# Optimization experiments

Measured on AMD Instinct MI355X. Metric: run time of the kernel, lower is better.

## Reference

```python
import jax, jax.numpy as jnp
import numpy as np

L, S, N, E = 1024, 1024, 16, 1024

def setup_inputs() -> dict:
    key = jax.random.key(0)
    ks = jax.random.split(key, 7)
    return {
        "query": jax.random.normal(ks[0], (L, N, E), dtype=jnp.float32),
        "key": jax.random.normal(ks[1], (S, N, E), dtype=jnp.float32),
        "value": jax.random.normal(ks[2], (S, N, E), dtype=jnp.float32),
        "q_proj_weight": jax.random.normal(ks[3], (E, E), dtype=jnp.float32) * (E ** -0.5),
        "k_proj_weight": jax.random.normal(ks[4], (E, E), dtype=jnp.float32) * (E ** -0.5),
        "v_proj_weight": jax.random.normal(ks[5], (E, E), dtype=jnp.float32) * (E ** -0.5),
        "in_proj_bias": jax.random.normal(ks[6], (3 * E,), dtype=jnp.float32) * 0.02,
    }

def reference(query, key, value, q_proj_weight, k_proj_weight, v_proj_weight, in_proj_bias):
    # query: (L, N, E); key/value: (S, N, E); single head => head_dim = E
    e = query.shape[-1]
    scaling = jnp.asarray(e, query.dtype) ** -0.5
    # F.linear(x, W, b) = x @ W.T + b
    q = (jnp.einsum("lne,fe->lnf", query, q_proj_weight) + in_proj_bias[:e]) * scaling
    k = jnp.einsum("sne,fe->snf", key, k_proj_weight) + in_proj_bias[e:2 * e]
    v = jnp.einsum("sne,fe->snf", value, v_proj_weight) + in_proj_bias[2 * e:]
    # scores: (N, L, S)
    scores = jnp.einsum("lne,sne->nls", q, k)
    attn = jax.nn.softmax(scores, axis=-1)
    # output back to (L, N, E)
    out = jnp.einsum("nls,sne->lne", attn, v)
    return out
```

## Files before the change

### kernel.cpp

```cpp
#include <hip/hip_runtime.h>
#include <stdint.h>


typedef __attribute__((ext_vector_type(8))) short bf16x8;
typedef __attribute__((ext_vector_type(4))) float f32x4;

__device__ __forceinline__ float bf2f(unsigned short u) {
    union { unsigned int i; float f; } w; w.i = ((unsigned int)u) << 16; return w.f;
}
__device__ __forceinline__ unsigned short f2bf(float f) {
    union { float f; unsigned int i; } w; w.f = f;
    unsigned int r = (w.i + 0x7FFFu + ((w.i >> 16) & 1u)) >> 16;
    return (unsigned short)r;
}

__device__ __forceinline__ void g2l16(const unsigned short* g, unsigned short* l) {
    __builtin_amdgcn_global_load_lds(
        (const __attribute__((address_space(1))) unsigned int*)g,
        (__attribute__((address_space(3))) unsigned int*)l, 16, 0, 0);
}

#define BM 256
#define BN 256
#define BK 32

template <int BIAS_MODE, typename OutT>
__global__ __launch_bounds__(512, 2) void gemm_bt2(
    const unsigned short* __restrict__ A,
    const unsigned short* __restrict__ B,
    OutT* __restrict__ C,
    const float* __restrict__ bias,
    float scale, int K,
    long lda, long ldb, long ldc,
    long aBatch, long bBatch, long cBatch,
    int gridM, int gridN)
{
    __shared__ __align__(16) unsigned short lds[65536];

    const int tid  = threadIdx.x;
    const int wave = tid >> 6;
    const int lane = tid & 63;
    const int lr   = lane & 15;
    const int q4   = lane >> 4;
    const int wm   = wave >> 2;
    const int wn   = wave & 3;

    const int p    = blockIdx.x;
    const int l    = ((p & 7) << 5) + (p >> 3);
    const int bcol = l % gridN;
    const int t2   = l / gridN;
    const int brow = t2 % gridM;
    const int bz   = t2 / gridM;

    const long m0 = (long)brow * BM;
    const long n0 = (long)bcol * BN;
    A += (long)bz * aBatch;
    B += (long)bz * bBatch;
    C += (long)bz * cBatch;

    const int tswz  = tid ^ ((tid >> 3) & 7);
    const int srow  = tswz >> 2;
    const int skoff = (tswz & 3) * 8;
    const unsigned short* aS0 = A + (m0 + srow) * lda + skoff;
    const unsigned short* aS1 = A + (m0 + 128 + srow) * lda + skoff;
    const unsigned short* bS0 = B + (n0 + srow) * ldb + skoff;
    const unsigned short* bS1 = B + (n0 + 128 + srow) * ldb + skoff;
    const int ldsW = wave * 512;

    const int myoff = (((lr << 2) | q4) ^ ((lr >> 1) & 7)) << 3;

    f32x4 acc[8][4];
    const f32x4 zero = {0.f, 0.f, 0.f, 0.f};
#pragma unroll
    for (int m = 0; m < 8; m++)
#pragma unroll
        for (int n = 0; n < 4; n++) acc[m][n] = zero;

    const int nkt = K / BK;

#pragma unroll
    for (int t = 0; t < 3; t++) {
        const long kb = (long)t * BK;
        unsigned short* base = &lds[t * 16384];
        g2l16(aS0 + kb, base + ldsW);
        g2l16(aS1 + kb, base + 4096 + ldsW);
        g2l16(bS0 + kb, base + 8192 + ldsW);
        g2l16(bS1 + kb, base + 12288 + ldsW);
    }
    asm volatile("s_waitcnt vmcnt(8)" ::: "memory");
    __builtin_amdgcn_s_barrier();

    for (int kt = 0; kt < nkt; kt++) {
        const int buf  = kt & 3;
        const int sbuf = (kt + 3) & 3;
        const int st   = (kt + 3 < nkt) ? kt + 3 : nkt - 1;
        const long kb  = (long)st * BK;
        const unsigned short* At = &lds[buf * 16384];
        const unsigned short* Bt = At + 8192;
        unsigned short* sb = &lds[sbuf * 16384];

        bf16x8 af[4], bfr[4];
#pragma unroll
        for (int m = 0; m < 4; m++)
            af[m] = *(const bf16x8*)&At[(wm * 128 + m * 16) * 32 + myoff];
#pragma unroll
        for (int n = 0; n < 4; n++)
            bfr[n] = *(const bf16x8*)&Bt[(wn * 64 + n * 16) * 32 + myoff];
        g2l16(aS0 + kb, sb + ldsW);
        g2l16(aS1 + kb, sb + 4096 + ldsW);
        __builtin_amdgcn_s_barrier();
        __builtin_amdgcn_s_setprio(1);
#pragma unroll
        for (int m = 0; m < 4; m++)
#pragma unroll
            for (int n = 0; n < 4; n++)
                acc[m][n] = __builtin_amdgcn_mfma_f32_16x16x32_bf16(
                    af[m], bfr[n], acc[m][n], 0, 0, 0);
        __builtin_amdgcn_s_setprio(0);
        __builtin_amdgcn_s_barrier();

        bf16x8 ag[4];
#pragma unroll
        for (int m = 0; m < 4; m++)
            ag[m] = *(const bf16x8*)&At[(wm * 128 + 64 + m * 16) * 32 + myoff];
        g2l16(bS0 + kb, sb + 8192 + ldsW);
        g2l16(bS1 + kb, sb + 12288 + ldsW);
        __builtin_amdgcn_s_barrier();
        __builtin_amdgcn_s_setprio(1);
#pragma unroll
        for (int m = 0; m < 4; m++)
#pragma unroll
            for (int n = 0; n < 4; n++)
                acc[4 + m][n] = __builtin_amdgcn_mfma_f32_16x16x32_bf16(
                    ag[m], bfr[n], acc[4 + m][n], 0, 0, 0);
        __builtin_amdgcn_s_setprio(0);
        asm volatile("s_waitcnt vmcnt(8)" ::: "memory");
        __builtin_amdgcn_s_barrier();
        __builtin_amdgcn_sched_barrier(0);
    }

    asm volatile("s_waitcnt vmcnt(0)" ::: "memory");
    __syncthreads();

    if constexpr (sizeof(OutT) == 2) {
#pragma unroll
        for (int m = 0; m < 8; m++)
#pragma unroll
            for (int n = 0; n < 4; n++) {
                const int col = wn * 64 + n * 16 + lr;
#pragma unroll
                for (int r = 0; r < 4; r++) {
                    const int row = wm * 128 + m * 16 + q4 * 4 + r;
                    float v = acc[m][n][r];
                    if constexpr (BIAS_MODE == 1) v += bias[n0 + col];
                    if constexpr (BIAS_MODE == 2) v += bias[m0 + row];
                    v *= scale;
                    lds[row * 256 + (col ^ (((row >> 2) & 3) << 4))] = f2bf(v);
                }
            }
        __syncthreads();
#pragma unroll
        for (int i = 0; i < 16; i++) {
            const int g   = i * 512 + tid;
            const int row = g >> 5;
            const int ch  = g & 31;
            bf16x8 v = *(const bf16x8*)&lds[row * 256 + ((ch * 8) ^ (((row >> 2) & 3) << 4))];
            *(bf16x8*)((unsigned short*)C + (m0 + row) * ldc + n0 + ch * 8) = v;
        }
    } else {
        float* fl = (float*)lds;
#pragma unroll
        for (int h = 0; h < 2; h++) {
            __syncthreads();
            if (wm == h) {
#pragma unroll
                for (int m = 0; m < 8; m++)
#pragma unroll
                    for (int n = 0; n < 4; n++) {
                        const int col = wn * 64 + n * 16 + lr;
#pragma unroll
                        for (int r = 0; r < 4; r++) {
                            const int rowh = m * 16 + q4 * 4 + r;
                            float v = acc[m][n][r];
                            if constexpr (BIAS_MODE == 1) v += bias[n0 + col];
                            if constexpr (BIAS_MODE == 2) v += bias[m0 + h * 128 + rowh];
                            v *= scale;
                            fl[rowh * 256 + (col ^ (((rowh >> 2) & 3) << 4))] = v;
                        }
                    }
            }
            __syncthreads();
#pragma unroll
            for (int i = 0; i < 16; i++) {
                const int g   = i * 512 + tid;
                const int row = g >> 6;
                const int ch  = g & 63;
                float4 v = *(const float4*)&fl[row * 256 + ((ch * 4) ^ (((row >> 2) & 3) << 4))];
                *(float4*)((float*)C + (m0 + h * 128 + row) * ldc + n0 + ch * 4) = v;
            }
        }
    }
}

__global__ __launch_bounds__(256) void cvt2_f32_bf16(
    const float* __restrict__ inA, unsigned short* __restrict__ outA, long n8A,
    const float* __restrict__ inB, unsigned short* __restrict__ outB, long n8B)
{
    const long total  = n8A + n8B;
    const long stride = (long)gridDim.x * blockDim.x;
    for (long i = (long)blockIdx.x * blockDim.x + threadIdx.x; i < total; i += stride) {
        const float* src;
        unsigned short* dst;
        long j;
        if (i < n8A) { src = inA; dst = outA; j = i; }
        else         { src = inB; dst = outB; j = i - n8A; }
        const float4* pp = (const float4*)(src + j * 8);
        float4 a = pp[0], b = pp[1];
        bf16x8 v;
        v[0] = (short)f2bf(a.x); v[1] = (short)f2bf(a.y);
        v[2] = (short)f2bf(a.z); v[3] = (short)f2bf(a.w);
        v[4] = (short)f2bf(b.x); v[5] = (short)f2bf(b.y);
        v[6] = (short)f2bf(b.z); v[7] = (short)f2bf(b.w);
        *(bf16x8*)(dst + j * 8) = v;
    }
}

__global__ __launch_bounds__(256) void softmax_rows(unsigned short* __restrict__ base)
{
    unsigned short* p = base + (long)blockIdx.x * 1024;
    const int tid = threadIdx.x;
    ushort4 u = ((const ushort4*)p)[tid];
    float x0 = bf2f(u.x), x1 = bf2f(u.y), x2 = bf2f(u.z), x3 = bf2f(u.w);
    x0 = fminf(fmaxf(x0, -1e30f), 1e30f);
    x1 = fminf(fmaxf(x1, -1e30f), 1e30f);
    x2 = fminf(fmaxf(x2, -1e30f), 1e30f);
    x3 = fminf(fmaxf(x3, -1e30f), 1e30f);

    float m = fmaxf(fmaxf(x0, x1), fmaxf(x2, x3));
#pragma unroll
    for (int o = 32; o > 0; o >>= 1) m = fmaxf(m, __shfl_xor(m, o));
    __shared__ float redm[4], reds[4];
    const int wave = tid >> 6, lane = tid & 63;
    if (lane == 0) redm[wave] = m;
    __syncthreads();
    m = fmaxf(fmaxf(redm[0], redm[1]), fmaxf(redm[2], redm[3]));

    float e0 = __expf(x0 - m), e1 = __expf(x1 - m);
    float e2 = __expf(x2 - m), e3 = __expf(x3 - m);
    float s = e0 + e1 + e2 + e3;
#pragma unroll
    for (int o = 32; o > 0; o >>= 1) s += __shfl_xor(s, o);
    if (lane == 0) reds[wave] = s;
    __syncthreads();
    s = reds[0] + reds[1] + reds[2] + reds[3];
    const float inv = 1.0f / s;

    ushort4 ov = make_ushort4(f2bf(e0 * inv), f2bf(e1 * inv),
                              f2bf(e2 * inv), f2bf(e3 * inv));
    ((ushort4*)p)[tid] = ov;
}

extern "C" void kernel_launch(void* const* d_in, const int* in_sizes, int n_in,
                              void* d_out, int out_size, void* d_ws, size_t ws_size,
                              hipStream_t stream) {
    const float* query = (const float*)d_in[0];
    const float* keyp  = (const float*)d_in[1];
    const float* valp  = (const float*)d_in[2];
    const float* wq    = (const float*)d_in[3];
    const float* wk    = (const float*)d_in[4];
    const float* wv    = (const float*)d_in[5];
    const float* bias  = (const float*)d_in[6];
    float* out = (float*)d_out;

    unsigned short* WSA = (unsigned short*)d_ws;
    unsigned short* WSB = WSA + 16777216;
    unsigned short* OC  = (unsigned short*)d_out;
    unsigned short* OD  = OC + 16777216;

    const dim3 cblk(256, 1, 1);
    const dim3 gblk(512, 1, 1);

    cvt2_f32_bf16<<<2048, cblk, 0, stream>>>(query, WSA, 2097152, wq, WSB, 131072);
    gemm_bt2<1, unsigned short><<<256, gblk, 0, stream>>>(
        WSA, WSB, OC, bias, 0.03125f, 1024,
        1024, 1024, 1024, 0, 0, 0, 64, 4);
    cvt2_f32_bf16<<<2048, cblk, 0, stream>>>(keyp, WSA, 2097152, wk, WSB, 131072);
    gemm_bt2<1, unsigned short><<<256, gblk, 0, stream>>>(
        WSA, WSB, OD, bias + 1024, 1.0f, 1024,
        1024, 1024, 1024, 0, 0, 0, 64, 4);
    gemm_bt2<0, unsigned short><<<256, gblk, 0, stream>>>(
        OC, OD, WSB, nullptr, 1.0f, 1024,
        16384, 16384, 1024, 1024, 1024, 1048576, 4, 4);
    softmax_rows<<<16384, cblk, 0, stream>>>(WSB);
    cvt2_f32_bf16<<<2048, cblk, 0, stream>>>(valp, OC, 2097152, wv, OD, 131072);
    gemm_bt2<2, unsigned short><<<256, gblk, 0, stream>>>(
        OD, OC, WSA, bias + 2048, 1.0f, 1024,
        1024, 16384, 1024, 0, 1024, 1048576, 4, 4);
    gemm_bt2<0, float><<<256, gblk, 0, stream>>>(
        WSB, WSA, out, nullptr, 1.0f, 1024,
        1024, 1024, 16384, 1048576, 1048576, 1024, 4, 4);
}
```

Baseline: 430.8 us.

## Double-buffer MFMA fragments in registers and use one barrier per k-tile

Restructures the GEMM main loop so the A/B fragments for the next k-tile are read from LDS into a second register set while the current tile's MFMAs run. The loop is unrolled by two and alternates between the two register sets. All four global-to-LDS loads for a stage are issued at the start of each step, and the wait count is tightened so only the newest stage can still be in flight. This cuts the per-tile barriers from three to one, aiming to reduce synchronization stalls and hide LDS latency behind MFMA work. The cost is more register pressure, and the unroll by two assumes an even number of k-tiles.

Measured after the change: 431.7 us. Within noise of the previous version (+0.2%).

```diff
diff --git a/kernel.cpp b/kernel.cpp
--- a/kernel.cpp
+++ b/kernel.cpp
@@ -87,57 +87,67 @@
         g2l16(bS0 + kb, base + 8192 + ldsW);
         g2l16(bS1 + kb, base + 12288 + ldsW);
     }
-    asm volatile("s_waitcnt vmcnt(8)" ::: "memory");
+    asm volatile("s_waitcnt vmcnt(4)" ::: "memory");
+    __builtin_amdgcn_sched_barrier(0);
     __builtin_amdgcn_s_barrier();
 
-    for (int kt = 0; kt < nkt; kt++) {
-        const int buf  = kt & 3;
-        const int sbuf = (kt + 3) & 3;
-        const int st   = (kt + 3 < nkt) ? kt + 3 : nkt - 1;
-        const long kb  = (long)st * BK;
-        const unsigned short* At = &lds[buf * 16384];
-        const unsigned short* Bt = At + 8192;
-        unsigned short* sb = &lds[sbuf * 16384];
-
-        bf16x8 af[4], bfr[4];
-#pragma unroll
-        for (int m = 0; m < 4; m++)
-            af[m] = *(const bf16x8*)&At[(wm * 128 + m * 16) * 32 + myoff];
-#pragma unroll
-        for (int n = 0; n < 4; n++)
-            bfr[n] = *(const bf16x8*)&Bt[(wn * 64 + n * 16) * 32 + myoff];
-        g2l16(aS0 + kb, sb + ldsW);
-        g2l16(aS1 + kb, sb + 4096 + ldsW);
-        __builtin_amdgcn_s_barrier();
-        __builtin_amdgcn_s_setprio(1);
-#pragma unroll
-        for (int m = 0; m < 4; m++)
-#pragma unroll
-            for (int n = 0; n < 4; n++)
-                acc[m][n] = __builtin_amdgcn_mfma_f32_16x16x32_bf16(
-                    af[m], bfr[n], acc[m][n], 0, 0, 0);
-        __builtin_amdgcn_s_setprio(0);
-        __builtin_amdgcn_s_barrier();
-
-        bf16x8 ag[4];
-#pragma unroll
-        for (int m = 0; m < 4; m++)
-            ag[m] = *(const bf16x8*)&At[(wm * 128 + 64 + m * 16) * 32 + myoff];
-        g2l16(bS0 + kb, sb + 8192 + ldsW);
-        g2l16(bS1 + kb, sb + 12288 + ldsW);
-        __builtin_amdgcn_s_barrier();
-        __builtin_amdgcn_s_setprio(1);
-#pragma unroll
-        for (int m = 0; m < 4; m++)
-#pragma unroll
-            for (int n = 0; n < 4; n++)
-                acc[4 + m][n] = __builtin_amdgcn_mfma_f32_16x16x32_bf16(
-                    ag[m], bfr[n], acc[4 + m][n], 0, 0, 0);
-        __builtin_amdgcn_s_setprio(0);
-        asm volatile("s_waitcnt vmcnt(8)" ::: "memory");
-        __builtin_amdgcn_s_barrier();
-        __builtin_amdgcn_sched_barrier(0);
-    }
+    bf16x8 afA[4], bfA[4], afB[4], bfB[4], ag[4];
+#pragma unroll
+    for (int m = 0; m < 4; m++)
+        afA[m] = *(const bf16x8*)&lds[(wm * 128 + m * 16) * 32 + myoff];
+#pragma unroll
+    for (int n = 0; n < 4; n++)
+        bfA[n] = *(const bf16x8*)&lds[8192 + (wn * 64 + n * 16) * 32 + myoff];
+
+#define TILE_STEP(KT, AC, BC, AN, BN)                                          \
+    {                                                                          \
+        const int kt_   = (KT);                                                \
+        const unsigned short* At = &lds[(kt_ & 3) * 16384];                    \
+        const unsigned short* Bt = At + 8192;                                  \
+        unsigned short* sb = &lds[((kt_ + 3) & 3) * 16384];                    \
+        const int st  = (kt_ + 3 < nkt) ? kt_ + 3 : nkt - 1;                   \
+        const long kb = (long)st * BK;                                         \
+        g2l16(aS0 + kb, sb + ldsW);                                            \
+        g2l16(aS1 + kb, sb + 4096 + ldsW);                                     \
+        g2l16(bS0 + kb, sb + 8192 + ldsW);                                     \
+        g2l16(bS1 + kb, sb + 12288 + ldsW);                                    \
+        _Pragma("unroll")                                                      \
+        for (int m = 0; m < 4; m++)                                            \
+            ag[m] = *(const bf16x8*)&At[(wm * 128 + 64 + m * 16) * 32 + myoff];\
+        __builtin_amdgcn_s_setprio(1);                                         \
+        _Pragma("unroll")                                                      \
+        for (int m = 0; m < 4; m++)                                            \
+            _Pragma("unroll")                                                  \
+            for (int n = 0; n < 4; n++)                                        \
+                acc[m][n] = __builtin_amdgcn_mfma_f32_16x16x32_bf16(           \
+                    AC[m], BC[n], acc[m][n], 0, 0, 0);                         \
+        __builtin_amdgcn_s_setprio(0);                                         \
+        const unsigned short* Atn = &lds[((kt_ + 1) & 3) * 16384];             \
+        const unsigned short* Btn = Atn + 8192;                                \
+        _Pragma("unroll")                                                      \
+        for (int m = 0; m < 4; m++)                                            \
+            AN[m] = *(const bf16x8*)&Atn[(wm * 128 + m * 16) * 32 + myoff];    \
+        _Pragma("unroll")                                                      \
+        for (int n = 0; n < 4; n++)                                            \
+            BN[n] = *(const bf16x8*)&Btn[(wn * 64 + n * 16) * 32 + myoff];     \
+        __builtin_amdgcn_s_setprio(1);                                         \
+        _Pragma("unroll")                                                      \
+        for (int m = 0; m < 4; m++)                                            \
+            _Pragma("unroll")                                                  \
+            for (int n = 0; n < 4; n++)                                        \
+                acc[4 + m][n] = __builtin_amdgcn_mfma_f32_16x16x32_bf16(       \
+                    ag[m], BC[n], acc[4 + m][n], 0, 0, 0);                     \
+        __builtin_amdgcn_s_setprio(0);                                         \
+        asm volatile("s_waitcnt vmcnt(4)" ::: "memory");                       \
+        __builtin_amdgcn_sched_barrier(0);                                     \
+        __builtin_amdgcn_s_barrier();                                          \
+    }
+
+    for (int kt = 0; kt < nkt; kt += 2) {
+        TILE_STEP(kt,     afA, bfA, afB, bfB);
+        TILE_STEP(kt + 1, afB, bfB, afA, bfA);
+    }
+#undef TILE_STEP
 
     asm volatile("s_waitcnt vmcnt(0)" ::: "memory");
     __syncthreads();
```

## Split GEMM tile across 16 waves with single-phase k-loop

Applied to the files above, without the earlier changes.

Doubles the GEMM workgroup to 1024 threads (16 waves), so each wave computes a 64x64 sub-tile instead of 128x64. Each thread now issues one A and one B async global-to-LDS copy per k-tile, and the two-phase k-loop with three barriers becomes a single MFMA phase with one barrier. The intent is more waves per CU to hide latency and fewer synchronisation points per iteration. In exchange, each wave reads more fragments from LDS per MFMA, and the launch bound of (1024, 4) may force a tight register budget that causes spills.

After: 425.7 us. No clear change (-1.2%).

```diff
diff --git a/kernel.cpp b/kernel.cpp
--- a/kernel.cpp
+++ b/kernel.cpp
@@ -25,7 +25,7 @@
 #define BK 32
 
 template <int BIAS_MODE, typename OutT>
-__global__ __launch_bounds__(512, 2) void gemm_bt2(
+__global__ __launch_bounds__(1024, 4) void gemm_bt2(
     const unsigned short* __restrict__ A,
     const unsigned short* __restrict__ B,
     OutT* __restrict__ C,
@@ -61,18 +61,16 @@
     const int tswz  = tid ^ ((tid >> 3) & 7);
     const int srow  = tswz >> 2;
     const int skoff = (tswz & 3) * 8;
-    const unsigned short* aS0 = A + (m0 + srow) * lda + skoff;
-    const unsigned short* aS1 = A + (m0 + 128 + srow) * lda + skoff;
-    const unsigned short* bS0 = B + (n0 + srow) * ldb + skoff;
-    const unsigned short* bS1 = B + (n0 + 128 + srow) * ldb + skoff;
+    const unsigned short* aS = A + (m0 + srow) * lda + skoff;
+    const unsigned short* bS = B + (n0 + srow) * ldb + skoff;
     const int ldsW = wave * 512;
 
     const int myoff = (((lr << 2) | q4) ^ ((lr >> 1) & 7)) << 3;
 
-    f32x4 acc[8][4];
+    f32x4 acc[4][4];
     const f32x4 zero = {0.f, 0.f, 0.f, 0.f};
 #pragma unroll
-    for (int m = 0; m < 8; m++)
+    for (int m = 0; m < 4; m++)
 #pragma unroll
         for (int n = 0; n < 4; n++) acc[m][n] = zero;
 
@@ -82,12 +80,11 @@
     for (int t = 0; t < 3; t++) {
         const long kb = (long)t * BK;
         unsigned short* base = &lds[t * 16384];
-        g2l16(aS0 + kb, base + ldsW);
-        g2l16(aS1 + kb, base + 4096 + ldsW);
-        g2l16(bS0 + kb, base + 8192 + ldsW);
-        g2l16(bS1 + kb, base + 12288 + ldsW);
-    }
-    asm volatile("s_waitcnt vmcnt(8)" ::: "memory");
+        g2l16(aS + kb, base + ldsW);
+        g2l16(bS + kb, base + 8192 + ldsW);
+    }
+    asm volatile("s_waitcnt vmcnt(4)" ::: "memory");
+    __builtin_amdgcn_sched_barrier(0);
     __builtin_amdgcn_s_barrier();
 
     for (int kt = 0; kt < nkt; kt++) {
@@ -99,16 +96,17 @@
         const unsigned short* Bt = At + 8192;
         unsigned short* sb = &lds[sbuf * 16384];
 
+        g2l16(aS + kb, sb + ldsW);
+        g2l16(bS + kb, sb + 8192 + ldsW);
+
         bf16x8 af[4], bfr[4];
 #pragma unroll
         for (int m = 0; m < 4; m++)
-            af[m] = *(const bf16x8*)&At[(wm * 128 + m * 16) * 32 + myoff];
+            af[m] = *(const bf16x8*)&At[(wm * 64 + m * 16) * 32 + myoff];
 #pragma unroll
         for (int n = 0; n < 4; n++)
             bfr[n] = *(const bf16x8*)&Bt[(wn * 64 + n * 16) * 32 + myoff];
-        g2l16(aS0 + kb, sb + ldsW);
-        g2l16(aS1 + kb, sb + 4096 + ldsW);
-        __builtin_amdgcn_s_barrier();
+
         __builtin_amdgcn_s_setprio(1);
 #pragma unroll
         for (int m = 0; m < 4; m++)
@@ -117,26 +115,10 @@
                 acc[m][n] = __builtin_amdgcn_mfma_f32_16x16x32_bf16(
                     af[m], bfr[n], acc[m][n], 0, 0, 0);
         __builtin_amdgcn_s_setprio(0);
+
+        asm volatile("s_waitcnt vmcnt(4)" ::: "memory");
+        __builtin_amdgcn_sched_barrier(0);
         __builtin_amdgcn_s_barrier();
-
-        bf16x8 ag[4];
-#pragma unroll
-        for (int m = 0; m < 4; m++)
-            ag[m] = *(const bf16x8*)&At[(wm * 128 + 64 + m * 16) * 32 + myoff];
-        g2l16(bS0 + kb, sb + 8192 + ldsW);
-        g2l16(bS1 + kb, sb + 12288 + ldsW);
-        __builtin_amdgcn_s_barrier();
-        __builtin_amdgcn_s_setprio(1);
-#pragma unroll
-        for (int m = 0; m < 4; m++)
-#pragma unroll
-            for (int n = 0; n < 4; n++)
-                acc[4 + m][n] = __builtin_amdgcn_mfma_f32_16x16x32_bf16(
-                    ag[m], bfr[n], acc[4 + m][n], 0, 0, 0);
-        __builtin_amdgcn_s_setprio(0);
-        asm volatile("s_waitcnt vmcnt(8)" ::: "memory");
-        __builtin_amdgcn_s_barrier();
-        __builtin_amdgcn_sched_barrier(0);
     }
 
     asm volatile("s_waitcnt vmcnt(0)" ::: "memory");
@@ -144,13 +126,13 @@
 
     if constexpr (sizeof(OutT) == 2) {
 #pragma unroll
-        for (int m = 0; m < 8; m++)
+        for (int m = 0; m < 4; m++)
 #pragma unroll
             for (int n = 0; n < 4; n++) {
                 const int col = wn * 64 + n * 16 + lr;
 #pragma unroll
                 for (int r = 0; r < 4; r++) {
-                    const int row = wm * 128 + m * 16 + q4 * 4 + r;
+                    const int row = wm * 64 + m * 16 + q4 * 4 + r;
                     float v = acc[m][n][r];
                     if constexpr (BIAS_MODE == 1) v += bias[n0 + col];
                     if constexpr (BIAS_MODE == 2) v += bias[m0 + row];
@@ -160,8 +142,8 @@
             }
         __syncthreads();
 #pragma unroll
-        for (int i = 0; i < 16; i++) {
-            const int g   = i * 512 + tid;
+        for (int i = 0; i < 8; i++) {
+            const int g   = i * 1024 + tid;
             const int row = g >> 5;
             const int ch  = g & 31;
             bf16x8 v = *(const bf16x8*)&lds[row * 256 + ((ch * 8) ^ (((row >> 2) & 3) << 4))];
@@ -172,15 +154,15 @@
 #pragma unroll
         for (int h = 0; h < 2; h++) {
             __syncthreads();
-            if (wm == h) {
-#pragma unroll
-                for (int m = 0; m < 8; m++)
+            if ((wm >> 1) == h) {
+#pragma unroll
+                for (int m = 0; m < 4; m++)
 #pragma unroll
                     for (int n = 0; n < 4; n++) {
                         const int col = wn * 64 + n * 16 + lr;
 #pragma unroll
                         for (int r = 0; r < 4; r++) {
-                            const int rowh = m * 16 + q4 * 4 + r;
+                            const int rowh = (wm & 1) * 64 + m * 16 + q4 * 4 + r;
                             float v = acc[m][n][r];
                             if constexpr (BIAS_MODE == 1) v += bias[n0 + col];
                             if constexpr (BIAS_MODE == 2) v += bias[m0 + h * 128 + rowh];
@@ -191,8 +173,8 @@
             }
             __syncthreads();
 #pragma unroll
-            for (int i = 0; i < 16; i++) {
-                const int g   = i * 512 + tid;
+            for (int i = 0; i < 8; i++) {
+                const int g   = i * 1024 + tid;
                 const int row = g >> 6;
                 const int ch  = g & 63;
                 float4 v = *(const float4*)&fl[row * 256 + ((ch * 4) ^ (((row >> 2) & 3) << 4))];
@@ -278,7 +260,7 @@
     unsigned short* OD  = OC + 16777216;
 
     const dim3 cblk(256, 1, 1);
-    const dim3 gblk(512, 1, 1);
+    const dim3 gblk(1024, 1, 1);
 
     cvt2_f32_bf16<<<2048, cblk, 0, stream>>>(query, WSA, 2097152, wq, WSB, 131072);
     gemm_bt2<1, unsigned short><<<256, gblk, 0, stream>>>(
```
